# Optimization experiments

Measured on AMD Instinct MI355X. Metric: run time of the kernel, lower is better.

## Reference

```python
import jax, jax.numpy as jnp
import numpy as np

B, C, F, J = 64, 16, 2048, 25
EMBED, CLASSES, NJ = 64, 5, 12
AFFECT = slice(0, 12)
UNAFFECT = slice(12, 24)


def setup_inputs() -> dict:
    key = jax.random.key(0)
    k0, k1, k2, k3 = jax.random.split(key, 4)
    features = jax.random.normal(k0, (B, C, F, J), dtype=jnp.float32)
    W1 = jax.random.normal(k1, (EMBED, C, NJ), dtype=jnp.float32) * 0.05
    b1 = jnp.zeros((EMBED,), jnp.float32)
    W2 = jax.random.normal(k2, (EMBED, C, NJ), dtype=jnp.float32) * 0.05
    b2 = jnp.zeros((EMBED,), jnp.float32)
    Wl = jax.random.normal(k3, (CLASSES, 16 * EMBED), dtype=jnp.float32) * 0.02
    bl = jnp.zeros((CLASSES,), jnp.float32)
    return {"features": features, "W1": W1, "b1": b1, "W2": W2, "b2": b2, "Wl": Wl, "bl": bl}


def _stat_features(x, proto):
    # x: [b, c, f, j]; single sort shared by min/max/quantiles/median
    f = x.shape[-2]
    xs = jnp.sort(x, axis=-2)

    def quant(p):
        # torch.quantile linear interpolation
        pos = p * (f - 1)
        lo = int(np.floor(pos)); hi = int(np.ceil(pos)); frac = np.float32(pos - lo)
        return xs[..., lo, :] * (1.0 - frac) + xs[..., hi, :] * frac

    s1 = xs[..., 0, :]                       # min
    s2 = xs[..., -1, :]                      # max
    s3 = quant(0.25)
    s4 = xs[..., (f - 1) // 2, :]            # torch.median: lower middle element
    s5 = quant(0.75)
    s6 = jnp.mean(x, axis=-2)
    s7 = jnp.std(x, axis=-2, ddof=1)         # torch.std unbiased
    s8 = s2 - s1
    z = (x - s6[..., None, :]) / s7[..., None, :]
    if proto:
        s9 = jnp.mean(z ** 3, axis=-2)       # skew
    else:
        s9 = jnp.mean(z ** 4, axis=-2) - 3.0  # excess kurtosis
    return jnp.stack([s2, s3, s4, s5, s6, s7, s8, s9], axis=-2)  # [b, c, 8, j]


def _fuse(stat, W, b):
    # Conv2d kernel (1, joints) == contraction over (c, j) per stat row
    out = jnp.einsum('bcsj,ecj->bes', stat, W) + b[None, :, None]
    return out.reshape(out.shape[0], -1)  # flatten (embed, stats) like torch.flatten


def reference(features, W1, b1, W2, b2, Wl, bl):
    affected = features[:, :, :, AFFECT]
    unaffected = features[:, :, :, UNAFFECT]
    stat_af = _stat_features(affected, proto=False)
    stat_ua = _stat_features(unaffected, proto=False)
    # attn=False path (STAT_VA block disabled)
    stat1 = _stat_features(unaffected + affected, proto=True)
    _ = _fuse(stat1, W1, b1)  # stat1 branch only feeds CL loss (get_cl_loss=False)
    stat2 = jnp.concatenate([stat_af, stat_ua], axis=-2)  # [b, c, 16, j]
    flat2 = _fuse(stat2, W2, b2)                          # [b, 16*embed]
    logits = flat2 @ Wl.T + bl
    return logits
```

## Files before the change

### kernel.cpp

```cpp
#include <hip/hip_runtime.h>
#include <hip/hip_bf16.h>
#include <math.h>


#define F_LEN 2048
#define JTOT 25
#define STATS_PER_BC 192
#define LP 2056

typedef float f4a __attribute__((ext_vector_type(4), aligned(4)));

__device__ __forceinline__ int swz(int i) {
  return (i & ~31) | ((i + ((i >> 5) << 2)) & 31);
}

template <int PAT>
__device__ __forceinline__ float ds_swz(float v) {
  return __int_as_float(
      __builtin_amdgcn_ds_swizzle(__float_as_int(v), PAT));
}
__device__ __forceinline__ float swzxor(float v, const int lm,
                                        const int addr32) {
  switch (lm) {
    case 1:  return ds_swz<0x041F>(v);
    case 2:  return ds_swz<0x081F>(v);
    case 4:  return ds_swz<0x101F>(v);
    case 8:  return ds_swz<0x201F>(v);
    case 16: return ds_swz<0x401F>(v);
    default: return __int_as_float(
        __builtin_amdgcn_ds_bpermute(addr32, __float_as_int(v)));
  }
}
__device__ __forceinline__ float wave_sum(float v, int addr32) {
  v += ds_swz<0x041F>(v);
  v += ds_swz<0x081F>(v);
  v += ds_swz<0x101F>(v);
  v += ds_swz<0x201F>(v);
  v += ds_swz<0x401F>(v);
  v += __int_as_float(
      __builtin_amdgcn_ds_bpermute(addr32, __float_as_int(v)));
  return v;
}

__device__ __forceinline__ void read_x(const float* wlds, int lane,
                                       float* x) {
  const float4* src4 = (const float4*)wlds;
#pragma unroll
  for (int q = 0; q < 8; ++q) {
    float4 v = src4[lane * 8 + ((lane + q) & 7)];
    x[4 * q] = v.x;
    x[4 * q + 1] = v.y;
    x[4 * q + 2] = v.z;
    x[4 * q + 3] = v.w;
  }
}

__global__ __launch_bounds__(256, 8) void stat_kernel(
    const float* __restrict__ Fp, float* __restrict__ stat2) {
  __shared__ float lds[2 * LP];
  const int g = blockIdx.x;
  const int xcd = g & 7;
  const int mm = g >> 3;
  const int bc = xcd * 128 + mm / 6;
  const int grp = mm % 6;
  const int t = threadIdx.x;
  const int w = t >> 6;
  const int lane = t & 63;
  const int addr32 = ((lane ^ 32) << 2);
  const int j0 = grp * 4;

  float vz[8], vw[8];
  const int rot = (t + ((t >> 5) << 2)) & 31;
  float* p0 = lds + (t & ~31) + rot;
  {
    const float* bbase = Fp + (size_t)bc * F_LEN * JTOT + j0;
#pragma unroll
    for (int it = 0; it < 8; ++it) {
      const int f = it * 256 + t;
      f4a v = *reinterpret_cast<const f4a*>(bbase + (size_t)f * JTOT);
      p0[it * 256] = v.x;
      p0[LP + it * 256] = v.y;
      vz[it] = v.z;
      vw[it] = v.w;
    }
  }
  __syncthreads();

  float x[32];
  if (w < 2) read_x(lds + w * LP, lane, x);
  __syncthreads();

  {
#pragma unroll
    for (int it = 0; it < 8; ++it) {
      p0[it * 256] = vz[it];
      p0[LP + it * 256] = vw[it];
    }
  }
  __syncthreads();
  if (w >= 2) read_x(lds + (w - 2) * LP, lane, x);

  float sum = 0.f;
#pragma unroll
  for (int e = 0; e < 32; ++e) sum += x[e];
  sum = wave_sum(sum, addr32);
  const float m = sum * (1.0f / 2048.0f);

  float c2 = 0.f, c4 = 0.f;
#pragma unroll
  for (int e = 0; e < 32; ++e) {
    float d = x[e] - m;
    float dd = d * d;
    c2 += dd;
    c4 += dd * dd;
  }
  c2 = wave_sum(c2, addr32);
  c4 = wave_sum(c4, addr32);
  const float var = c2 * (1.0f / 2047.0f);
  const float sd = sqrtf(var);
  const float kurt = (c4 * (1.0f / 2048.0f)) / (var * var) - 3.0f;

#pragma unroll
  for (int kp = 1; kp <= 4; ++kp) {
    const int k = 1 << kp;
#pragma unroll
    for (int jp = kp - 1; jp >= 0; --jp) {
      const int st = 1 << jp;
#pragma unroll
      for (int e = 0; e < 32; ++e) {
        if ((e & st) == 0) {
          const bool up = ((e & k) == 0);
          float a = x[e], b = x[e + st];
          float lo2 = fminf(a, b), hi2 = fmaxf(a, b);
          x[e] = up ? lo2 : hi2;
          x[e + st] = up ? hi2 : lo2;
        }
      }
    }
  }

  unsigned Fst = 0u;
#pragma unroll
  for (int kp = 5; kp <= 11; ++kp) {
    const unsigned d = ((lane >> (kp - 5)) & 1) ? 0x80000000u : 0u;
#pragma unroll
    for (int jp = kp - 1; jp >= 5; --jp) {
      const int lm = 1 << (jp - 5);
      const unsigned r = ((lane >> (jp - 5)) & 1) ? 0x80000000u : 0u;
      const unsigned tgt = d ^ r;
      const unsigned fl = tgt ^ Fst;
      Fst = tgt;
#pragma unroll
      for (int e = 0; e < 32; ++e)
        x[e] = __uint_as_float(__float_as_uint(x[e]) ^ fl);
#pragma unroll
      for (int e = 0; e < 32; ++e) {
        float o = swzxor(x[e], lm, addr32);
        x[e] = fminf(x[e], -o);
      }
    }
    {
      const unsigned fl = d ^ Fst;
      Fst = d;
#pragma unroll
      for (int e = 0; e < 32; ++e)
        x[e] = __uint_as_float(__float_as_uint(x[e]) ^ fl);
    }
#pragma unroll
    for (int jp = 4; jp >= 0; --jp) {
      const int st = 1 << jp;
#pragma unroll
      for (int e = 0; e < 32; ++e) {
        if ((e & st) == 0) {
          float a = x[e], b = x[e + st];
          x[e] = fminf(a, b);
          x[e + st] = fmaxf(a, b);
        }
      }
    }
  }

  const float mn = __shfl(x[0], 0, 64);
  const float a511 = __shfl(x[31], 15, 64);
  const float a512 = __shfl(x[0], 16, 64);
  const float amed = __shfl(x[31], 31, 64);
  const float a1535 = __shfl(x[31], 47, 64);
  const float a1536 = __shfl(x[0], 48, 64);
  const float mx = __shfl(x[31], 63, 64);

  if (lane == 0) {
    const float q25 = 0.25f * a511 + 0.75f * a512;
    const float q75 = 0.75f * a1535 + 0.25f * a1536;
    const int j = j0 + w;
    const int jj = (j < 12) ? j : j - 12;
    const int sb = (j < 12) ? 0 : 8;
    float st8[8] = {mx, q25, amed, q75, m, sd, mx - mn, kurt};
    float* o = stat2 + (bc * 16 + sb) * 12 + jj;
#pragma unroll
    for (int s2 = 0; s2 < 8; ++s2) o[s2 * 12] = st8[s2];
  }
}

__global__ __launch_bounds__(256) void fuse_kernel(
    const float* __restrict__ stat2, const float* __restrict__ W2,
    const float* __restrict__ b2, const float* __restrict__ Wl,
    const float* __restrict__ bl, float* __restrict__ out) {
  __shared__ float s_stat[16 * STATS_PER_BC];
  __shared__ float s_flat[1024];
  __shared__ float s_red[4];

  const int b = blockIdx.x;
  const int t = threadIdx.x;

  for (int idx = t; idx < 16 * STATS_PER_BC; idx += 256)
    s_stat[idx] = stat2[b * (16 * STATS_PER_BC) + idx];
  __syncthreads();

  const int e = t & 63;
  const int q = t >> 6;
  float acc[4] = {0.f, 0.f, 0.f, 0.f};
  for (int c = 0; c < 16; ++c) {
    const float* wrow = W2 + (e * 16 + c) * 12;
    const float* srow = s_stat + c * STATS_PER_BC;
#pragma unroll
    for (int jj = 0; jj < 12; ++jj) {
      const float wv = wrow[jj];
#pragma unroll
      for (int ss = 0; ss < 4; ++ss)
        acc[ss] += srow[(q * 4 + ss) * 12 + jj] * wv;
    }
  }
  const float bb = b2[e];
#pragma unroll
  for (int ss = 0; ss < 4; ++ss)
    s_flat[e * 16 + q * 4 + ss] = acc[ss] + bb;
  __syncthreads();

  for (int k = 0; k < 5; ++k) {
    float p = 0.f;
    for (int i = t; i < 1024; i += 256) p += s_flat[i] * Wl[k * 1024 + i];
#pragma unroll
    for (int off = 32; off; off >>= 1) p += __shfl_down(p, off, 64);
    if ((t & 63) == 0) s_red[t >> 6] = p;
    __syncthreads();
    if (t == 0)
      out[b * 5 + k] = s_red[0] + s_red[1] + s_red[2] + s_red[3] + bl[k];
    __syncthreads();
  }
}

extern "C" void kernel_launch(void* const* d_in, const int* in_sizes, int n_in,
                              void* d_out, int out_size, void* d_ws,
                              size_t ws_size, hipStream_t stream) {
  const float* Fp = (const float*)d_in[0];
  const float* W2 = (const float*)d_in[3];
  const float* b2 = (const float*)d_in[4];
  const float* Wl = (const float*)d_in[5];
  const float* bl = (const float*)d_in[6];
  float* out = (float*)d_out;

  float* stat2 = (float*)d_ws;

  stat_kernel<<<6144, 256, 0, stream>>>(Fp, stat2);
  fuse_kernel<<<64, 256, 0, stream>>>(stat2, W2, b2, Wl, bl, out);
}
```

Measured before the change: 462.7 us.

## Precompose conv and linear weights, use DPP lane exchanges, relax launch bounds

Folds W2 and Wl into one combined matrix M (5x3072) and a bias vector C in a new prep kernel. The final stage then becomes one dot product per batch row instead of a conv followed by a linear layer. It also swaps the ds_swizzle-based xor-partner exchanges for DPP row operations where possible, in both the bitonic sort and the wave reductions. The min-waves hint of 8 is dropped from stat_kernel's launch bounds, which may change register allocation and occupancy. The price is an extra kernel launch, and the sum order changes, so float rounding differs.

```diff
diff --git a/kernel.cpp b/kernel.cpp
--- a/kernel.cpp
+++ b/kernel.cpp
@@ -10,35 +10,47 @@
 
 typedef float f4a __attribute__((ext_vector_type(4), aligned(4)));
 
-__device__ __forceinline__ int swz(int i) {
-  return (i & ~31) | ((i + ((i >> 5) << 2)) & 31);
-}
-
 template <int PAT>
 __device__ __forceinline__ float ds_swz(float v) {
   return __int_as_float(
       __builtin_amdgcn_ds_swizzle(__float_as_int(v), PAT));
 }
-__device__ __forceinline__ float swzxor(float v, const int lm,
-                                        const int addr32) {
+
+template <int CTRL, int BANK>
+__device__ __forceinline__ int upd_dpp(int old_, int src) {
+  return __builtin_amdgcn_update_dpp(old_, src, CTRL, 0xF, BANK, false);
+}
+
+__device__ __forceinline__ float xpartner(float v, const int lm,
+                                          const int addr32) {
+  const int vi = __float_as_int(v);
   switch (lm) {
-    case 1:  return ds_swz<0x041F>(v);
-    case 2:  return ds_swz<0x081F>(v);
-    case 4:  return ds_swz<0x101F>(v);
-    case 8:  return ds_swz<0x201F>(v);
-    case 16: return ds_swz<0x401F>(v);
-    default: return __int_as_float(
-        __builtin_amdgcn_ds_bpermute(addr32, __float_as_int(v)));
-  }
-}
+    case 1:
+      return __int_as_float(upd_dpp<0xB1, 0xF>(vi, vi));
+    case 2:
+      return __int_as_float(upd_dpp<0x4E, 0xF>(vi, vi));
+    case 4: {
+      const int t1 = upd_dpp<0x104, 0x5>(vi, vi);
+      const int t2 = upd_dpp<0x114, 0xA>(t1, vi);
+      return __int_as_float(t2);
+    }
+    case 8:
+      return __int_as_float(upd_dpp<0x128, 0xF>(vi, vi));
+    case 16:
+      return ds_swz<0x401F>(v);
+    default:
+      return __int_as_float(
+          __builtin_amdgcn_ds_bpermute(addr32, vi));
+  }
+}
+
 __device__ __forceinline__ float wave_sum(float v, int addr32) {
-  v += ds_swz<0x041F>(v);
-  v += ds_swz<0x081F>(v);
-  v += ds_swz<0x101F>(v);
-  v += ds_swz<0x201F>(v);
-  v += ds_swz<0x401F>(v);
-  v += __int_as_float(
-      __builtin_amdgcn_ds_bpermute(addr32, __float_as_int(v)));
+  v += xpartner(v, 1, addr32);
+  v += xpartner(v, 2, addr32);
+  v += xpartner(v, 4, addr32);
+  v += xpartner(v, 8, addr32);
+  v += xpartner(v, 16, addr32);
+  v += xpartner(v, 32, addr32);
   return v;
 }
 
@@ -55,7 +67,7 @@
   }
 }
 
-__global__ __launch_bounds__(256, 8) void stat_kernel(
+__global__ __launch_bounds__(256) void stat_kernel(
     const float* __restrict__ Fp, float* __restrict__ stat2) {
   __shared__ float lds[2 * LP];
   const int g = blockIdx.x;
@@ -155,7 +167,7 @@
         x[e] = __uint_as_float(__float_as_uint(x[e]) ^ fl);
 #pragma unroll
       for (int e = 0; e < 32; ++e) {
-        float o = swzxor(x[e], lm, addr32);
+        float o = xpartner(x[e], lm, addr32);
         x[e] = fminf(x[e], -o);
       }
     }
@@ -201,52 +213,67 @@
   }
 }
 
-__global__ __launch_bounds__(256) void fuse_kernel(
-    const float* __restrict__ stat2, const float* __restrict__ W2,
-    const float* __restrict__ b2, const float* __restrict__ Wl,
-    const float* __restrict__ bl, float* __restrict__ out) {
-  __shared__ float s_stat[16 * STATS_PER_BC];
-  __shared__ float s_flat[1024];
-  __shared__ float s_red[4];
-
+__global__ __launch_bounds__(256) void prep_kernel(
+    const float* __restrict__ W2, const float* __restrict__ b2,
+    const float* __restrict__ Wl, const float* __restrict__ bl,
+    float* __restrict__ M, float* __restrict__ C) {
+  const int g = blockIdx.x;
+  const int t = threadIdx.x;
+  if (g < 60) {
+    const int id = g * 256 + t;
+    const int k = id / 3072;
+    const int r = id % 3072;
+    const int c = r / 192;
+    const int s = (r % 192) / 12;
+    const int j = r % 12;
+    const float* wl = Wl + k * 1024 + s;
+    const float* w2 = W2 + c * 12 + j;
+    float acc = 0.f;
+#pragma unroll 8
+    for (int e = 0; e < 64; ++e) acc += wl[e * 16] * w2[e * 192];
+    M[id] = acc;
+  } else if (t < 64) {
+    const int e = t;
+    const int addr32 = ((e ^ 32) << 2);
+    for (int k = 0; k < 5; ++k) {
+      const float* wl = Wl + k * 1024 + e * 16;
+      float rs = 0.f;
+#pragma unroll
+      for (int s = 0; s < 16; ++s) rs += wl[s];
+      float v = wave_sum(rs * b2[e], addr32);
+      if (e == 0) C[k] = v + bl[k];
+    }
+  }
+}
+
+__global__ __launch_bounds__(256) void logits_kernel(
+    const float* __restrict__ stat2, const float* __restrict__ M,
+    const float* __restrict__ C, float* __restrict__ out) {
+  __shared__ float s_red[20];
   const int b = blockIdx.x;
   const int t = threadIdx.x;
-
-  for (int idx = t; idx < 16 * STATS_PER_BC; idx += 256)
-    s_stat[idx] = stat2[b * (16 * STATS_PER_BC) + idx];
-  __syncthreads();
-
-  const int e = t & 63;
-  const int q = t >> 6;
-  float acc[4] = {0.f, 0.f, 0.f, 0.f};
-  for (int c = 0; c < 16; ++c) {
-    const float* wrow = W2 + (e * 16 + c) * 12;
-    const float* srow = s_stat + c * STATS_PER_BC;
-#pragma unroll
-    for (int jj = 0; jj < 12; ++jj) {
-      const float wv = wrow[jj];
-#pragma unroll
-      for (int ss = 0; ss < 4; ++ss)
-        acc[ss] += srow[(q * 4 + ss) * 12 + jj] * wv;
-    }
-  }
-  const float bb = b2[e];
-#pragma unroll
-  for (int ss = 0; ss < 4; ++ss)
-    s_flat[e * 16 + q * 4 + ss] = acc[ss] + bb;
-  __syncthreads();
-
-  for (int k = 0; k < 5; ++k) {
-    float p = 0.f;
-    for (int i = t; i < 1024; i += 256) p += s_flat[i] * Wl[k * 1024 + i];
-#pragma unroll
-    for (int off = 32; off; off >>= 1) p += __shfl_down(p, off, 64);
-    if ((t & 63) == 0) s_red[t >> 6] = p;
-    __syncthreads();
-    if (t == 0)
-      out[b * 5 + k] = s_red[0] + s_red[1] + s_red[2] + s_red[3] + bl[k];
-    __syncthreads();
-  }
+  const int lane = t & 63;
+  const int w = t >> 6;
+  const int addr32 = ((lane ^ 32) << 2);
+
+  float acc[5] = {0.f, 0.f, 0.f, 0.f, 0.f};
+#pragma unroll
+  for (int ii = 0; ii < 12; ++ii) {
+    const int i = ii * 256 + t;
+    const float s = stat2[b * 3072 + i];
+#pragma unroll
+    for (int k = 0; k < 5; ++k) acc[k] += s * M[k * 3072 + i];
+  }
+#pragma unroll
+  for (int k = 0; k < 5; ++k) acc[k] = wave_sum(acc[k], addr32);
+  if (lane == 0) {
+#pragma unroll
+    for (int k = 0; k < 5; ++k) s_red[w * 5 + k] = acc[k];
+  }
+  __syncthreads();
+  if (t < 5)
+    out[b * 5 + t] =
+        s_red[t] + s_red[5 + t] + s_red[10 + t] + s_red[15 + t] + C[t];
 }
 
 extern "C" void kernel_launch(void* const* d_in, const int* in_sizes, int n_in,
@@ -260,7 +287,10 @@
   float* out = (float*)d_out;
 
   float* stat2 = (float*)d_ws;
-
+  float* M = stat2 + 196608;
+  float* C = M + 15360;
+
+  prep_kernel<<<61, 256, 0, stream>>>(W2, b2, Wl, bl, M, C);
   stat_kernel<<<6144, 256, 0, stream>>>(Fp, stat2);
-  fuse_kernel<<<64, 256, 0, stream>>>(stat2, W2, b2, Wl, bl, out);
-}
+  logits_kernel<<<64, 256, 0, stream>>>(stat2, M, C, out);
+}
```

Measured after the change: 461.7 us. No clear change (-0.2%).
